# Performance work log

Hardware: AMD Instinct MI355X
Metric: run time of the kernel (lower is better)

## Reference

```python
import jax, jax.numpy as jnp
import numpy as np

B, N, C = 8, 1024, 768
H = 12
HD = C // H
FF = 2048
NUM_CLASSES = 1000
SCALE = HD ** -0.5


def layer_norm(x, g, b, eps=1e-5):
    mu = jnp.mean(x, axis=-1, keepdims=True)
    var = jnp.var(x, axis=-1, keepdims=True)
    return (x - mu) * jax.lax.rsqrt(var + eps) * g + b


def setup_inputs() -> dict:
    key = jax.random.key(0)
    ks = jax.random.split(key, 12)
    s = lambda *sh: 0.02
    return {
        "src": jax.random.normal(ks[0], (B, N, C), jnp.float32),
        "y": jax.random.uniform(ks[1], (B, NUM_CLASSES), jnp.float32),
        "scorenet_h_src": jax.random.normal(ks[2], (B, NUM_CLASSES), jnp.float32),
        "pre_g": jnp.ones((C,), jnp.float32),
        "pre_b": jnp.zeros((C,), jnp.float32),
        "qkv_w": jax.random.normal(ks[3], (C, 3 * C), jnp.float32) * 0.02,
        "proj_w": jax.random.normal(ks[4], (C, C), jnp.float32) * 0.02,
        "proj_b": jnp.zeros((C,), jnp.float32),
        "n1_g": jnp.ones((C,), jnp.float32),
        "n1_b": jnp.zeros((C,), jnp.float32),
        "l1_w": jax.random.normal(ks[5], (C, FF), jnp.float32) * 0.02,
        "l1_b": jnp.zeros((FF,), jnp.float32),
        "l2_w": jax.random.normal(ks[6], (FF, C), jnp.float32) * 0.02,
        "l2_b": jnp.zeros((C,), jnp.float32),
    }


def attention(x, qkv_w, proj_w, proj_b):
    # x: [B, N, C] -> qkv: [B, N, 3, H, HD]
    qkv = (x @ qkv_w).reshape(B, N, 3, H, HD)
    qkv = jnp.transpose(qkv, (2, 0, 3, 1, 4))  # [3, B, H, N, HD]
    q, k, v = qkv[0], qkv[1], qkv[2]
    attn = jax.nn.softmax(jnp.einsum("bhqd,bhkd->bhqk", q, k) * SCALE, axis=-1)
    out = jnp.einsum("bhqk,bhkd->bhqd", attn, v)  # [B, H, N, HD]
    out = jnp.transpose(out, (0, 2, 1, 3)).reshape(B, N, C)
    out = out @ proj_w + proj_b
    return out, attn


def reference(src, y, scorenet_h_src, pre_g, pre_b, qkv_w, proj_w, proj_b,
              n1_g, n1_b, l1_w, l1_b, l2_w, l2_b):
    # eval-mode forward: dropout / drop_path are identity, mixup branches off
    x, attn = attention(layer_norm(src, pre_g, pre_b), qkv_w, proj_w, proj_b)
    src = src + x
    src_n = layer_norm(src, n1_g, n1_b)
    ffn = jax.nn.gelu(src_n @ l1_w + l1_b, approximate=False) @ l2_w + l2_b
    src = src_n + ffn
    return (src, scorenet_h_src, y, attn)
```

## Files before the change

kernel.cpp:

```cpp
#include <hip/hip_runtime.h>
#include <stdint.h>

typedef unsigned short u16;
typedef __bf16 bf16x8 __attribute__((ext_vector_type(8)));
typedef float f32x4 __attribute__((ext_vector_type(4)));


__device__ __forceinline__ u16 f2bf(float f) {
  union { float f; unsigned u; } v; v.f = f;
  unsigned r = v.u + 0x7fffu + ((v.u >> 16) & 1u);
  return (u16)(r >> 16);
}
__device__ __forceinline__ float bf2f(unsigned u) {
  union { unsigned u; float f; } v; v.u = u << 16; return v.f;
}

__device__ __forceinline__ void async16(const void* g, void* l) {
  __builtin_amdgcn_global_load_lds(
      (const __attribute__((address_space(1))) void*)g,
      (__attribute__((address_space(3))) void*)l, 16, 0, 0);
}

__device__ __forceinline__ f32x4 mfma16(bf16x8 a, bf16x8 b, f32x4 c) {
  return __builtin_amdgcn_mfma_f32_16x16x32_bf16(a, b, c, 0, 0, 0);
}

__device__ __forceinline__ float gelu_exact(float x) {
  return 0.5f * x * (1.0f + erff(x * 0.70710678118654752440f));
}

__global__ __launch_bounds__(256) void ln_kernel(
    const float* __restrict__ x, const float* __restrict__ g,
    const float* __restrict__ b, u16* __restrict__ obf,
    float* __restrict__ of) {
  const size_t row = blockIdx.x;
  const float* xr = x + row * 768;
  const int t = threadIdx.x;
  const int w = t >> 6, lane = t & 63;
  float v0 = xr[t], v1 = xr[t + 256], v2 = xr[t + 512];
  float s = v0 + v1 + v2;
  float sq = v0 * v0 + v1 * v1 + v2 * v2;
#pragma unroll
  for (int off = 32; off > 0; off >>= 1) {
    s += __shfl_down(s, off);
    sq += __shfl_down(sq, off);
  }
  __shared__ float ss[4], ssq[4];
  if (lane == 0) { ss[w] = s; ssq[w] = sq; }
  __syncthreads();
  s = ss[0] + ss[1] + ss[2] + ss[3];
  sq = ssq[0] + ssq[1] + ssq[2] + ssq[3];
  const float mean = s * (1.0f / 768.0f);
  const float var = sq * (1.0f / 768.0f) - mean * mean;
  const float rstd = rsqrtf(var + 1e-5f);
  float y0 = (v0 - mean) * rstd * g[t] + b[t];
  float y1 = (v1 - mean) * rstd * g[t + 256] + b[t + 256];
  float y2 = (v2 - mean) * rstd * g[t + 512] + b[t + 512];
  obf[row * 768 + t] = f2bf(y0);
  obf[row * 768 + t + 256] = f2bf(y1);
  obf[row * 768 + t + 512] = f2bf(y2);
  if (of) {
    of[row * 768 + t] = y0;
    of[row * 768 + t + 256] = y1;
    of[row * 768 + t + 512] = y2;
  }
}

__device__ __forceinline__ void transpose_tile(float (*tile)[33],
                                               const float* __restrict__ W,
                                               u16* __restrict__ Wt, int K,
                                               int N, int bx, int by) {
  const int n0 = bx * 32, k0 = by * 32;
  const int tx = threadIdx.x, ty = threadIdx.y;
  for (int r = ty; r < 32; r += 8)
    tile[r][tx] = W[(size_t)(k0 + r) * N + n0 + tx];
  __syncthreads();
  for (int r = ty; r < 32; r += 8)
    Wt[(size_t)(n0 + r) * K + k0 + tx] = f2bf(tile[tx][r]);
}

__global__ void misc_kernel(const float* __restrict__ qkv_w,
                            const float* __restrict__ proj_w,
                            const float* __restrict__ l1_w,
                            const float* __restrict__ l2_w,
                            u16* __restrict__ qkvwT, u16* __restrict__ projwT,
                            u16* __restrict__ l1wT, u16* __restrict__ l2wT,
                            const float* __restrict__ y,
                            const float* __restrict__ sc,
                            float* __restrict__ out) {
  __shared__ float tile[32][33];
  int bid = blockIdx.x;
  if (bid < 1728) { transpose_tile(tile, qkv_w, qkvwT, 768, 2304, bid % 72, bid / 72); return; }
  bid -= 1728;
  if (bid < 576) { transpose_tile(tile, proj_w, projwT, 768, 768, bid % 24, bid / 24); return; }
  bid -= 576;
  if (bid < 1536) { transpose_tile(tile, l1_w, l1wT, 768, 2048, bid % 64, bid / 64); return; }
  bid -= 1536;
  if (bid < 1536) { transpose_tile(tile, l2_w, l2wT, 2048, 768, bid % 24, bid / 24); return; }
  bid -= 1536;
  const int t = threadIdx.y * 32 + threadIdx.x;
  const int i = bid * 256 + t;
  if (i < 8000) {
    out[6291456 + i] = sc[i];
    out[6299456 + i] = y[i];
  }
}

__global__ void vt_kernel(const u16* __restrict__ qkv, u16* __restrict__ vt) {
  const int bh = blockIdx.z, b = bh / 12, h = bh % 12;
  const int n0 = blockIdx.x * 32, d0 = blockIdx.y * 32;
  __shared__ u16 tile[32][33];
  const u16* Vp = qkv + (size_t)b * 1024 * 2304 + 1536 + h * 64;
  const int tx = threadIdx.x, ty = threadIdx.y;
  for (int r = ty; r < 32; r += 8)
    tile[r][tx] = Vp[(size_t)(n0 + r) * 2304 + d0 + tx];
  __syncthreads();
  u16* Op = vt + (size_t)bh * 64 * 1024;
  for (int r = ty; r < 32; r += 8)
    Op[(size_t)(d0 + r) * 1024 + n0 + tx] = tile[tx][r];
}

template <int BM, int BN, int GN, int WM, int WN>
__global__ __launch_bounds__(256) void gemm_kernel(
    const u16* __restrict__ A, int lda, const u16* __restrict__ Bt, int ldb,
    const float* __restrict__ bias, const float* __restrict__ res,
    float* __restrict__ outF, u16* __restrict__ outB, int ldc, int K,
    int act) {
  __shared__ u16 As[2][BM * 32];
  __shared__ u16 Bs[2][BN * 32];
  const int tid = threadIdx.x;
  const int w = tid >> 6, lane = tid & 63;
  const size_t mBase = (size_t)blockIdx.y * BM;
  const size_t nBase = (size_t)blockIdx.x * BN;
  const int rq = lane >> 2;
  const int k8 = (lane & 3) * 8;
  const int wmBase = (w / GN) * (WM * 16);
  const int wnBase = (w % GN) * (WN * 16);
  const int tm = lane & 15, kq = lane >> 4;
  const f32x4 zero = {0.f, 0.f, 0.f, 0.f};
  f32x4 acc[WM][WN];
#pragma unroll
  for (int i = 0; i < WM; i++)
#pragma unroll
    for (int j = 0; j < WN; j++) acc[i][j] = zero;

#pragma unroll
  for (int c = w; c < BM / 16; c += 4)
    async16(A + (mBase + c * 16 + rq) * lda + k8, &As[0][c * 16 * 32]);
#pragma unroll
  for (int c = w; c < BN / 16; c += 4)
    async16(Bt + (nBase + c * 16 + rq) * ldb + k8, &Bs[0][c * 16 * 32]);

  int cur = 0;
  for (int kt = 0; kt < K; kt += 32) {
    __syncthreads();
    if (kt + 32 < K) {
      const int nxt = cur ^ 1;
#pragma unroll
      for (int c = w; c < BM / 16; c += 4)
        async16(A + (mBase + c * 16 + rq) * lda + kt + 32 + k8,
                &As[nxt][c * 16 * 32]);
#pragma unroll
      for (int c = w; c < BN / 16; c += 4)
        async16(Bt + (nBase + c * 16 + rq) * ldb + kt + 32 + k8,
                &Bs[nxt][c * 16 * 32]);
    }
    bf16x8 af[WM], bfv[WN];
#pragma unroll
    for (int i = 0; i < WM; i++)
      af[i] = *(const bf16x8*)&As[cur][(wmBase + i * 16 + tm) * 32 + kq * 8];
#pragma unroll
    for (int j = 0; j < WN; j++)
      bfv[j] = *(const bf16x8*)&Bs[cur][(wnBase + j * 16 + tm) * 32 + kq * 8];
#pragma unroll
    for (int i = 0; i < WM; i++)
#pragma unroll
      for (int j = 0; j < WN; j++) acc[i][j] = mfma16(af[i], bfv[j], acc[i][j]);
    cur ^= 1;
  }

#pragma unroll
  for (int i = 0; i < WM; i++) {
    const size_t row0 = mBase + wmBase + i * 16 + kq * 4;
#pragma unroll
    for (int j = 0; j < WN; j++) {
      const size_t col = nBase + wnBase + j * 16 + tm;
      const float bv = bias ? bias[col] : 0.0f;
#pragma unroll
      for (int r = 0; r < 4; r++) {
        const size_t rr = row0 + r;
        float v = acc[i][j][r] + bv;
        if (act) v = gelu_exact(v);
        if (res) v += res[rr * ldc + col];
        if (outF) outF[rr * ldc + col] = v;
        if (outB) outB[rr * ldc + col] = f2bf(v);
      }
    }
  }
}

__global__ __launch_bounds__(256, 3) void flash_kernel(
    const u16* __restrict__ qkv, const u16* __restrict__ vt,
    float* __restrict__ attn, u16* __restrict__ aout) {
  __shared__ u16 Qs[32 * 64];
  __shared__ u16 KV[2 * 128 * 64];
  __shared__ u16 Ps[32 * 128];
  __shared__ float psum[4][32];
  __shared__ float rinv[32];
  const int tid = threadIdx.x;
  const int w = tid >> 6, lane = tid & 63;
  const int tm = lane & 15, kq = lane >> 4;
  const int bh = blockIdx.y, b = bh / 12, h = bh % 12;
  const size_t m0 = (size_t)blockIdx.x * 32;
  const u16* Qp = qkv + (size_t)b * 1024 * 2304 + h * 64;
  const u16* Kp = Qp + 768;
  const u16* Vp = vt + (size_t)bh * 64 * 1024;
  float* Ab = attn + ((size_t)bh * 1024 + m0) * 1024;

  {
    const int r = tid >> 3, c = tid & 7;
    *(uint4*)&Qs[r * 64 + ((c ^ (r & 7)) * 8)] =
        *(const uint4*)(Qp + (m0 + r) * 2304 + c * 8);
  }
  __syncthreads();
  bf16x8 aq[2][2];
#pragma unroll
  for (int i = 0; i < 2; i++)
#pragma unroll
    for (int k2 = 0; k2 < 2; k2++) {
      const int m = i * 16 + tm;
      aq[i][k2] =
          *(const bf16x8*)&Qs[m * 64 + (((k2 * 4 + kq) ^ (m & 7)) * 8)];
    }

  f32x4 rs[2] = {{0.f, 0.f, 0.f, 0.f}, {0.f, 0.f, 0.f, 0.f}};
  for (int cc = 0; cc < 4; ++cc) {
    const int nc = cc * 256;
    __syncthreads();
#pragma unroll
    for (int u = 0; u < 8; ++u) {
      const int idx = u * 256 + tid;
      const int r = idx >> 3, c = idx & 7;
      *(uint4*)&KV[r * 64 + ((c ^ (r & 7)) * 8)] =
          *(const uint4*)(Kp + (size_t)(nc + r) * 2304 + c * 8);
    }
    __syncthreads();
#pragma unroll
    for (int jj = 0; jj < 4; ++jj) {
      const int n = (w * 4 + jj) * 16 + tm;
      bf16x8 bk[2];
#pragma unroll
      for (int k2 = 0; k2 < 2; k2++)
        bk[k2] =
            *(const bf16x8*)&KV[n * 64 + (((k2 * 4 + kq) ^ (n & 7)) * 8)];
#pragma unroll
      for (int i = 0; i < 2; i++) {
        f32x4 s = {0.f, 0.f, 0.f, 0.f};
        s = mfma16(aq[i][0], bk[0], s);
        s = mfma16(aq[i][1], bk[1], s);
#pragma unroll
        for (int r = 0; r < 4; r++) rs[i][r] += __expf(s[r] * 0.125f);
      }
    }
  }
#pragma unroll
  for (int i = 0; i < 2; i++)
#pragma unroll
    for (int r = 0; r < 4; r++) {
      float v = rs[i][r];
      v += __shfl_xor(v, 1); v += __shfl_xor(v, 2);
      v += __shfl_xor(v, 4); v += __shfl_xor(v, 8);
      if (tm == 0) psum[w][i * 16 + kq * 4 + r] = v;
    }
  __syncthreads();
  if (tid < 32)
    rinv[tid] =
        1.0f / (psum[0][tid] + psum[1][tid] + psum[2][tid] + psum[3][tid]);

  const f32x4 zero = {0.f, 0.f, 0.f, 0.f};
  f32x4 oacc[2] = {zero, zero};
  const int mi = w & 1, dp = w >> 1;
  for (int cc = 0; cc < 8; ++cc) {
    const int nc = cc * 128;
    __syncthreads();
#pragma unroll
    for (int u = 0; u < 4; ++u) {
      const int idx = u * 256 + tid;
      const int r = idx >> 3, c = idx & 7;
      *(uint4*)&KV[r * 64 + ((c ^ (r & 7)) * 8)] =
          *(const uint4*)(Kp + (size_t)(nc + r) * 2304 + c * 8);
    }
#pragma unroll
    for (int u = 0; u < 4; ++u) {
      const int idx = u * 256 + tid;
      const int d = idx >> 4, c = idx & 15;
      *(uint4*)&KV[8192 + d * 128 + ((c ^ (d & 15)) * 8)] =
          *(const uint4*)(Vp + (size_t)d * 1024 + nc + c * 8);
    }
    __syncthreads();
#pragma unroll
    for (int jj = 0; jj < 2; ++jj) {
      const int nb = w * 2 + jj;
      const int n = nb * 16 + tm;
      bf16x8 bk[2];
#pragma unroll
      for (int k2 = 0; k2 < 2; k2++)
        bk[k2] =
            *(const bf16x8*)&KV[n * 64 + (((k2 * 4 + kq) ^ (n & 7)) * 8)];
#pragma unroll
      for (int i = 0; i < 2; i++) {
        f32x4 s = {0.f, 0.f, 0.f, 0.f};
        s = mfma16(aq[i][0], bk[0], s);
        s = mfma16(aq[i][1], bk[1], s);
        const int row = i * 16 + kq * 4;
#pragma unroll
        for (int r = 0; r < 4; r++) {
          const float p = __expf(s[r] * 0.125f) * rinv[row + r];
          Ab[(size_t)(row + r) * 1024 + nc + nb * 16 + tm] = p;
          const int pr = row + r, pn = nb * 16 + tm;
          Ps[pr * 128 + (((pn >> 3) ^ (pr & 7)) * 8) + (pn & 7)] = f2bf(p);
        }
      }
    }
    __syncthreads();
#pragma unroll
    for (int k2 = 0; k2 < 4; ++k2) {
      const int m = mi * 16 + tm;
      const bf16x8 ap =
          *(const bf16x8*)&Ps[m * 128 + (((k2 * 4 + kq) ^ (m & 7)) * 8)];
#pragma unroll
      for (int jd = 0; jd < 2; ++jd) {
        const int d = dp * 32 + jd * 16 + tm;
        const bf16x8 bv = *(const bf16x8*)&KV[8192 + d * 128 +
                                              (((k2 * 4 + kq) ^ (d & 15)) * 8)];
        oacc[jd] = mfma16(ap, bv, oacc[jd]);
      }
    }
  }
#pragma unroll
  for (int jd = 0; jd < 2; ++jd)
#pragma unroll
    for (int r = 0; r < 4; ++r) {
      const size_t gm = (size_t)b * 1024 + m0 + mi * 16 + kq * 4 + r;
      aout[gm * 768 + h * 64 + dp * 32 + jd * 16 + tm] = f2bf(oacc[jd][r]);
    }
}

extern "C" void kernel_launch(void* const* d_in, const int* in_sizes, int n_in,
                              void* d_out, int out_size, void* d_ws,
                              size_t ws_size, hipStream_t stream) {
  const float* src    = (const float*)d_in[0];
  const float* yin    = (const float*)d_in[1];
  const float* scin   = (const float*)d_in[2];
  const float* pre_g  = (const float*)d_in[3];
  const float* pre_b  = (const float*)d_in[4];
  const float* qkv_w  = (const float*)d_in[5];
  const float* proj_w = (const float*)d_in[6];
  const float* proj_b = (const float*)d_in[7];
  const float* n1_g   = (const float*)d_in[8];
  const float* n1_b   = (const float*)d_in[9];
  const float* l1_w   = (const float*)d_in[10];
  const float* l1_b   = (const float*)d_in[11];
  const float* l2_w   = (const float*)d_in[12];
  const float* l2_b   = (const float*)d_in[13];
  float* outp = (float*)d_out;
  float* attn = outp + 6307456;

  char* ws = (char*)d_ws;
  u16* qkvwT  = (u16*)(ws + 0ull);
  u16* projwT = (u16*)(ws + 3538944ull);
  u16* l1wT   = (u16*)(ws + 4718592ull);
  u16* l2wT   = (u16*)(ws + 7864320ull);
  const size_t P0 = 11010048ull;
  u16* xn   = (u16*)(ws + P0);
  u16* qkv  = (u16*)(ws + P0 + 12582912ull);
  u16* vt   = (u16*)(ws + P0 + 50331648ull);
  u16* aout = (u16*)(ws + P0 + 62914560ull);
  float* src2 = (float*)(ws + P0);
  u16*  snb   = (u16*)(ws + P0 + 25165824ull);
  u16*  hbuf  = (u16*)(ws + P0 + 37748736ull);
  float* snf  = (float*)(ws + P0 + 71303168ull);

  dim3 tb(32, 8);
  misc_kernel<<<5439, tb, 0, stream>>>(qkv_w, proj_w, l1_w, l2_w, qkvwT,
                                       projwT, l1wT, l2wT, yin, scin, outp);
  ln_kernel<<<8192, 256, 0, stream>>>(src, pre_g, pre_b, xn, nullptr);
  gemm_kernel<128, 128, 2, 4, 4><<<dim3(18, 64), 256, 0, stream>>>(
      xn, 768, qkvwT, 768, nullptr, nullptr, nullptr, qkv, 2304, 768, 0);
  vt_kernel<<<dim3(32, 2, 96), tb, 0, stream>>>(qkv, vt);
  flash_kernel<<<dim3(32, 96), 256, 0, stream>>>(qkv, vt, attn, aout);
  gemm_kernel<64, 128, 4, 4, 2><<<dim3(6, 128), 256, 0, stream>>>(
      aout, 768, projwT, 768, proj_b, src, src2, nullptr, 768, 768, 0);
  ln_kernel<<<8192, 256, 0, stream>>>(src2, n1_g, n1_b, snb, snf);
  gemm_kernel<128, 128, 2, 4, 4><<<dim3(16, 64), 256, 0, stream>>>(
      snb, 768, l1wT, 768, l1_b, nullptr, nullptr, hbuf, 2048, 768, 1);
  gemm_kernel<64, 128, 4, 4, 2><<<dim3(6, 128), 256, 0, stream>>>(
      hbuf, 2048, l2wT, 2048, l2_b, snf, outp, nullptr, 768, 2048, 0);
}
```

Measured before the change: 821.2 us.

## Add 256x256-tile 8-wave GEMM with staged async loads for QKV and FFN1

```diff
diff --git a/kernel.cpp b/kernel.cpp
--- a/kernel.cpp
+++ b/kernel.cpp
@@ -28,6 +28,11 @@
 __device__ __forceinline__ float gelu_exact(float x) {
   return 0.5f * x * (1.0f + erff(x * 0.70710678118654752440f));
 }
+
+#define VMCNT(n) asm volatile("s_waitcnt vmcnt(" #n ")" ::: "memory")
+#define LGKM0 asm volatile("s_waitcnt lgkmcnt(0)" ::: "memory")
+#define SCHED0 __builtin_amdgcn_sched_barrier(0)
+#define BAR __builtin_amdgcn_s_barrier()
 
 __global__ __launch_bounds__(256) void ln_kernel(
     const float* __restrict__ x, const float* __restrict__ g,
@@ -199,6 +204,118 @@
   }
 }
 
+#define QUAD(P)                                                              \
+  __builtin_amdgcn_s_setprio(1);                                             \
+  _Pragma("unroll") for (int i2 = 0; i2 < 2; ++i2) {                         \
+    _Pragma("unroll") for (int j = 0; j < 4; ++j) {                          \
+      acc[(P)*2 + i2][j] = mfma16(aF[i2][0], bF[j][0], acc[(P)*2 + i2][j]);  \
+      acc[(P)*2 + i2][j] = mfma16(aF[i2][1], bF[j][1], acc[(P)*2 + i2][j]);  \
+    }                                                                        \
+  }                                                                          \
+  __builtin_amdgcn_s_setprio(0);
+
+template <int ACT>
+__global__ __launch_bounds__(512, 2) void gemm256_kernel(
+    const u16* __restrict__ A, int lda, const u16* __restrict__ Bt, int ldb,
+    const float* __restrict__ bias, u16* __restrict__ outB, int ldc, int K,
+    int NX, int nwg8) {
+  __shared__ u16 As[2][256 * 64];
+  __shared__ u16 Bs[2][256 * 64];
+  const int tid = threadIdx.x;
+  const int w = tid >> 6, lane = tid & 63;
+  const int wr = w >> 2, wc = w & 3;
+  const int tm = lane & 15, kq = lane >> 4;
+  const int id = blockIdx.x;
+  const int wg = (id & 7) * nwg8 + (id >> 3);
+  const size_t mBase = (size_t)(wg / NX) * 256;
+  const size_t nBase = (size_t)(wg % NX) * 256;
+  const int srow = tid >> 3;
+  const int gch = (tid & 7) ^ (srow & 7);
+
+#define STAGE_B(buf, kt, rb)                                          \
+  async16(Bt + (nBase + (rb) + srow) * (size_t)ldb + (kt) + gch * 8,  \
+          &Bs[buf][(rb) * 64 + tid * 8])
+#define STAGE_A(buf, kt, rb)                                          \
+  async16(A + (mBase + (rb) + srow) * (size_t)lda + (kt) + gch * 8,   \
+          &As[buf][(rb) * 64 + tid * 8])
+
+  f32x4 acc[8][4];
+  const f32x4 zero = {0.f, 0.f, 0.f, 0.f};
+#pragma unroll
+  for (int i = 0; i < 8; ++i)
+#pragma unroll
+    for (int j = 0; j < 4; ++j) acc[i][j] = zero;
+
+  auto rdA = [&](int buf, int i, int s) -> bf16x8 {
+    const int rl = wr * 128 + i * 16 + tm;
+    const int ch = (s * 4 + kq) ^ (rl & 7);
+    return *(const bf16x8*)&As[buf][rl * 64 + ch * 8];
+  };
+  auto rdB = [&](int buf, int j, int s) -> bf16x8 {
+    const int rl = wc * 64 + j * 16 + tm;
+    const int ch = (s * 4 + kq) ^ (rl & 7);
+    return *(const bf16x8*)&Bs[buf][rl * 64 + ch * 8];
+  };
+
+  STAGE_B(0, 0, 0); STAGE_B(0, 0, 64); STAGE_B(0, 0, 128); STAGE_B(0, 0, 192);
+  STAGE_A(0, 0, 0); STAGE_A(0, 0, 128); STAGE_A(0, 0, 64); STAGE_A(0, 0, 192);
+  VMCNT(2);
+  BAR;
+
+  const int T = K >> 6;
+  bf16x8 bF[4][2], aF[2][2];
+  for (int t = 0; t < T; ++t) {
+    const int cur = t & 1, nxt = cur ^ 1;
+    const int kt1 = (t + 1) << 6;
+    const bool last = (t == T - 1);
+#pragma unroll
+    for (int j = 0; j < 4; ++j) { bF[j][0] = rdB(cur, j, 0); bF[j][1] = rdB(cur, j, 1); }
+    aF[0][0] = rdA(cur, 0, 0); aF[0][1] = rdA(cur, 0, 1);
+    aF[1][0] = rdA(cur, 1, 0); aF[1][1] = rdA(cur, 1, 1);
+    if (!last) { STAGE_B(nxt, kt1, 0); STAGE_B(nxt, kt1, 64); }
+    BAR; LGKM0; SCHED0;
+    QUAD(0);
+    BAR;
+    aF[0][0] = rdA(cur, 2, 0); aF[0][1] = rdA(cur, 2, 1);
+    aF[1][0] = rdA(cur, 3, 0); aF[1][1] = rdA(cur, 3, 1);
+    if (!last) { STAGE_B(nxt, kt1, 128); STAGE_B(nxt, kt1, 192); VMCNT(4); }
+    else { VMCNT(0); }
+    BAR; LGKM0; SCHED0;
+    QUAD(1);
+    BAR;
+    aF[0][0] = rdA(cur, 4, 0); aF[0][1] = rdA(cur, 4, 1);
+    aF[1][0] = rdA(cur, 5, 0); aF[1][1] = rdA(cur, 5, 1);
+    if (!last) { STAGE_A(nxt, kt1, 0); STAGE_A(nxt, kt1, 128); }
+    BAR; LGKM0; SCHED0;
+    QUAD(2);
+    BAR;
+    aF[0][0] = rdA(cur, 6, 0); aF[0][1] = rdA(cur, 6, 1);
+    aF[1][0] = rdA(cur, 7, 0); aF[1][1] = rdA(cur, 7, 1);
+    if (!last) { STAGE_A(nxt, kt1, 64); STAGE_A(nxt, kt1, 192); VMCNT(2); }
+    BAR; LGKM0; SCHED0;
+    QUAD(3);
+    BAR;
+  }
+
+#pragma unroll
+  for (int i = 0; i < 8; ++i) {
+    const size_t row0 = mBase + wr * 128 + i * 16 + kq * 4;
+#pragma unroll
+    for (int j = 0; j < 4; ++j) {
+      const size_t col = nBase + wc * 64 + j * 16 + tm;
+      const float bv = bias ? bias[col] : 0.0f;
+#pragma unroll
+      for (int r = 0; r < 4; ++r) {
+        float v = acc[i][j][r] + bv;
+        if (ACT) v = gelu_exact(v);
+        outB[(row0 + r) * ldc + col] = f2bf(v);
+      }
+    }
+  }
+#undef STAGE_A
+#undef STAGE_B
+}
+
 __global__ __launch_bounds__(256, 3) void flash_kernel(
     const u16* __restrict__ qkv, const u16* __restrict__ vt,
     float* __restrict__ attn, u16* __restrict__ aout) {
@@ -385,15 +502,15 @@
   misc_kernel<<<5439, tb, 0, stream>>>(qkv_w, proj_w, l1_w, l2_w, qkvwT,
                                        projwT, l1wT, l2wT, yin, scin, outp);
   ln_kernel<<<8192, 256, 0, stream>>>(src, pre_g, pre_b, xn, nullptr);
-  gemm_kernel<128, 128, 2, 4, 4><<<dim3(18, 64), 256, 0, stream>>>(
-      xn, 768, qkvwT, 768, nullptr, nullptr, nullptr, qkv, 2304, 768, 0);
+  gemm256_kernel<0><<<288, 512, 0, stream>>>(xn, 768, qkvwT, 768, nullptr,
+                                             qkv, 2304, 768, 9, 36);
   vt_kernel<<<dim3(32, 2, 96), tb, 0, stream>>>(qkv, vt);
   flash_kernel<<<dim3(32, 96), 256, 0, stream>>>(qkv, vt, attn, aout);
   gemm_kernel<64, 128, 4, 4, 2><<<dim3(6, 128), 256, 0, stream>>>(
       aout, 768, projwT, 768, proj_b, src, src2, nullptr, 768, 768, 0);
   ln_kernel<<<8192, 256, 0, stream>>>(src2, n1_g, n1_b, snb, snf);
-  gemm_kernel<128, 128, 2, 4, 4><<<dim3(16, 64), 256, 0, stream>>>(
-      snb, 768, l1wT, 768, l1_b, nullptr, nullptr, hbuf, 2048, 768, 1);
+  gemm256_kernel<1><<<256, 512, 0, stream>>>(snb, 768, l1wT, 768, l1_b,
+                                             hbuf, 2048, 768, 8, 32);
   gemm_kernel<64, 128, 4, 4, 2><<<dim3(6, 128), 256, 0, stream>>>(
       hbuf, 2048, l2wT, 2048, l2_b, snf, outp, nullptr, 768, 2048, 0);
 }
```

New measurement: 807.1 us. No clear change (-1.7%).
